# Performance work log

Hardware: AMD Instinct MI355X
Metric: run time of the kernel (lower is better)

## Reference

```python
import jax, jax.numpy as jnp
import numpy as np

B, T, C, V = 8, 2048, 1024, 32000


def setup_inputs() -> dict:
    key = jax.random.key(0)
    ks = jax.random.split(key, 12)
    s = 1.0 / np.sqrt(C)
    return {
        "input_tokens": jax.random.randint(ks[0], (B, T), 0, V),
        "xx_init": jnp.zeros((B, C), jnp.float32),
        "aa_init": jnp.zeros((B, C), jnp.float32),
        "bb_init": jnp.zeros((B, C), jnp.float32),
        "pp_init": jnp.zeros((B, C), jnp.float32),  # with aa=bb=0 this is equivalent to -inf init
        "emb": jax.random.normal(ks[1], (V, C), jnp.float32) * 0.02,
        "time_mix_k": jax.random.uniform(ks[2], (C,), jnp.float32),
        "time_mix_v": jax.random.uniform(ks[3], (C,), jnp.float32),
        "time_mix_r": jax.random.uniform(ks[4], (C,), jnp.float32),
        "time_decay": jax.random.normal(ks[5], (C,), jnp.float32) * 0.1,
        "time_first": jax.random.normal(ks[6], (C,), jnp.float32) * 0.1,
        "Wk": jax.random.normal(ks[7], (C, C), jnp.float32) * s,
        "Wv": jax.random.normal(ks[8], (C, C), jnp.float32) * s,
        "Wr": jax.random.normal(ks[9], (C, C), jnp.float32) * s,
        "Wo": jax.random.normal(ks[10], (C, C), jnp.float32) * s,
    }


def _wkv_scan(k, v, aa0, bb0, pp0, w, u):
    """Numerically-stable RWKV WKV recurrence.
    k, v: [T, B, C]; aa0/bb0/pp0: [B, C]; w (decay, negative), u (bonus): [C]."""
    def step(carry, kv):
        aa, bb, pp = carry
        kt, vt = kv
        ww = u + kt
        p = jnp.maximum(pp, ww)
        e1 = jnp.exp(pp - p)
        e2 = jnp.exp(ww - p)
        wkv = (e1 * aa + e2 * vt) / (e1 * bb + e2)
        ww2 = pp + w
        p2 = jnp.maximum(ww2, kt)
        e1b = jnp.exp(ww2 - p2)
        e2b = jnp.exp(kt - p2)
        return (e1b * aa + e2b * vt, e1b * bb + e2b, p2), wkv
    (aa, bb, pp), out = jax.lax.scan(step, (aa0, bb0, pp0), (k, v))
    return out, aa, bb, pp


def _forward(input_tokens, xx_init, aa_init, bb_init, pp_init, emb,
             time_mix_k, time_mix_v, time_mix_r, time_decay, time_first,
             Wk, Wv, Wr, Wo):
    x = emb[input_tokens]                                   # [B, T, C]
    xprev = jnp.concatenate([xx_init[:, None, :], x[:, :-1]], axis=1)  # token shift
    xk = x * time_mix_k + xprev * (1.0 - time_mix_k)
    xv = x * time_mix_v + xprev * (1.0 - time_mix_v)
    xr = x * time_mix_r + xprev * (1.0 - time_mix_r)
    k = jnp.einsum("btc,dc->btd", xk, Wk)
    v = jnp.einsum("btc,dc->btd", xv, Wv)
    r = jax.nn.sigmoid(jnp.einsum("btc,dc->btd", xr, Wr))
    w = -jnp.exp(time_decay)                                # per-channel decay
    u = time_first
    wkv, _, _, _ = _wkv_scan(jnp.swapaxes(k, 0, 1), jnp.swapaxes(v, 0, 1),
                             aa_init, bb_init, pp_init, w, u)
    wkv = jnp.swapaxes(wkv, 0, 1)                           # [B, T, C]
    rwkv = jnp.einsum("btc,dc->btd", r * wkv, Wo)
    e1 = rwkv[:, -1]          # final-step state
    e2 = rwkv.mean(axis=1)    # time-averaged state
    hx = (e1 + e2) * 0.5
    return jnp.stack([hx, hx])  # (hx, cx) stacked -> [2, B, C]


def reference(input_tokens, xx_init, aa_init, bb_init, pp_init, emb,
              time_mix_k, time_mix_v, time_mix_r, time_decay, time_first,
              Wk, Wv, Wr, Wo):
    return _forward(input_tokens, xx_init, aa_init, bb_init, pp_init, emb,
                    time_mix_k, time_mix_v, time_mix_r, time_decay, time_first,
                    Wk, Wv, Wr, Wo)
```

## Files before the change

kernel.cpp:

```cpp
#include <hip/hip_runtime.h>

#define Bdim 8
#define Tdim 2048
#define Cdim 1024
#define CHUNK 128
#define NCHUNK 16
#define BC (Bdim*Cdim)

typedef float floatx4 __attribute__((ext_vector_type(4)));
typedef _Float16 half8 __attribute__((ext_vector_type(8)));
typedef _Float16 half4v __attribute__((ext_vector_type(4)));

__device__ __forceinline__ void load16(const void* g, void* l) {
    __builtin_amdgcn_global_load_lds(
        (const __attribute__((address_space(1))) void*)g,
        (__attribute__((address_space(3))) void*)l, 16, 0, 0);
}

__global__ __launch_bounds__(256) void embed_mix(const int* __restrict__ tokens,
                                                 const float* __restrict__ xx_init,
                                                 const float* __restrict__ emb,
                                                 _Float16* __restrict__ xe) {
    int row = blockIdx.x;
    int b = row / (Tdim + 1);
    int tt = row % (Tdim + 1);
    const float* src;
    if (tt == 0) src = xx_init + (size_t)b * Cdim;
    else         src = emb + (size_t)tokens[b * Tdim + tt - 1] * Cdim;
    int c0 = threadIdx.x * 4;
    float4 f = *reinterpret_cast<const float4*>(src + c0);
    half4v h;
    h[0] = (_Float16)f.x; h[1] = (_Float16)f.y; h[2] = (_Float16)f.z; h[3] = (_Float16)f.w;
    *reinterpret_cast<half4v*>(xe + (size_t)row * Cdim + c0) = h;
}

__global__ __launch_bounds__(256) void mix3(const _Float16* __restrict__ xe,
                                            const float* __restrict__ tmk,
                                            const float* __restrict__ tmv,
                                            const float* __restrict__ tmr,
                                            _Float16* __restrict__ xk,
                                            _Float16* __restrict__ xv,
                                            _Float16* __restrict__ xr) {
    int row = blockIdx.x;
    int b = row >> 11;
    int t = row & (Tdim - 1);
    const _Float16* cur = xe + ((size_t)(b * (Tdim + 1) + t + 1)) * Cdim;
    const _Float16* prv = cur - Cdim;
    int c = threadIdx.x * 4;
    half4v cu = *reinterpret_cast<const half4v*>(cur + c);
    half4v pv = *reinterpret_cast<const half4v*>(prv + c);
    float4 mk = *reinterpret_cast<const float4*>(tmk + c);
    float4 mv = *reinterpret_cast<const float4*>(tmv + c);
    float4 mr = *reinterpret_cast<const float4*>(tmr + c);
    half4v hk, hv, hr;
    float cf[4] = {(float)cu[0], (float)cu[1], (float)cu[2], (float)cu[3]};
    float pf[4] = {(float)pv[0], (float)pv[1], (float)pv[2], (float)pv[3]};
    float mkf[4] = {mk.x, mk.y, mk.z, mk.w};
    float mvf[4] = {mv.x, mv.y, mv.z, mv.w};
    float mrf[4] = {mr.x, mr.y, mr.z, mr.w};
    #pragma unroll
    for (int j = 0; j < 4; j++) {
        hk[j] = (_Float16)(mkf[j] * cf[j] + (1.0f - mkf[j]) * pf[j]);
        hv[j] = (_Float16)(mvf[j] * cf[j] + (1.0f - mvf[j]) * pf[j]);
        hr[j] = (_Float16)(mrf[j] * cf[j] + (1.0f - mrf[j]) * pf[j]);
    }
    size_t o = (size_t)row * Cdim + c;
    *reinterpret_cast<half4v*>(xk + o) = hk;
    *reinterpret_cast<half4v*>(xv + o) = hv;
    *reinterpret_cast<half4v*>(xr + o) = hr;
}

__global__ __launch_bounds__(256) void wconv(const float* __restrict__ Wk,
                                             const float* __restrict__ Wv,
                                             const float* __restrict__ Wr,
                                             _Float16* __restrict__ Wh) {
    const float* W = blockIdx.y == 0 ? Wk : (blockIdx.y == 1 ? Wv : Wr);
    _Float16* dst = Wh + (size_t)blockIdx.y * Cdim * Cdim;
    int i = (blockIdx.x * 256 + threadIdx.x) * 4;
    float4 f = *reinterpret_cast<const float4*>(W + i);
    half4v h;
    h[0] = (_Float16)f.x; h[1] = (_Float16)f.y; h[2] = (_Float16)f.z; h[3] = (_Float16)f.w;
    *reinterpret_cast<half4v*>(dst + i) = h;
}

__global__ __launch_bounds__(256) void gemm_kvr(const _Float16* __restrict__ xk,
                                                const _Float16* __restrict__ xv,
                                                const _Float16* __restrict__ xr,
                                                const _Float16* __restrict__ Wh,
                                                _Float16* __restrict__ ko,
                                                _Float16* __restrict__ vo,
                                                _Float16* __restrict__ ro) {
    const int which = blockIdx.y;
    const _Float16* X = which == 0 ? xk : (which == 1 ? xv : xr);
    const _Float16* W = Wh + (size_t)which * Cdim * Cdim;
    _Float16* out     = which == 0 ? ko : (which == 1 ? vo : ro);

    const int lin = blockIdx.x;
    const int xcd = lin & 7;
    const int loc = lin >> 3;
    const int mt = xcd * 16 + (loc >> 3);
    const int nt = loc & 7;
    const int m0 = mt * 128;
    const int n0 = nt * 128;

    __shared__ _Float16 As[128 * 64];
    __shared__ _Float16 Bs[128 * 64];

    const int tid = threadIdx.x;
    const int lane = tid & 63;
    const int wave = tid >> 6;
    const int wm = (wave >> 1) * 64;
    const int wn = (wave & 1) * 64;
    const int lr = lane & 15;
    const int lk = lane >> 4;

    const _Float16* Asrc = X + (size_t)m0 * Cdim;
    const _Float16* Bsrc = W + (size_t)n0 * Cdim;

    floatx4 acc[4][4] = {};

    for (int k0 = 0; k0 < Cdim; k0 += 64) {
        #pragma unroll
        for (int i = 0; i < 4; i++) {
            int e = i * 256 + tid;
            int r = e >> 3;
            int cbp = e & 7;
            int cbl = cbp ^ (r & 7);
            load16(Asrc + (size_t)r * Cdim + k0 + cbl * 8, (char*)As + e * 16);
            load16(Bsrc + (size_t)r * Cdim + k0 + cbl * 8, (char*)Bs + e * 16);
        }
        __syncthreads();
        #pragma unroll
        for (int kk = 0; kk < 64; kk += 32) {
            const int kb_ = kk >> 3;
            half8 af[4], bf[4];
            #pragma unroll
            for (int mi = 0; mi < 4; mi++) {
                int r = wm + mi * 16 + lr;
                int cb = (kb_ + lk) ^ (r & 7);
                af[mi] = *reinterpret_cast<const half8*>(As + r * 64 + cb * 8);
            }
            #pragma unroll
            for (int ni = 0; ni < 4; ni++) {
                int r = wn + ni * 16 + lr;
                int cb = (kb_ + lk) ^ (r & 7);
                bf[ni] = *reinterpret_cast<const half8*>(Bs + r * 64 + cb * 8);
            }
            #pragma unroll
            for (int mi = 0; mi < 4; mi++)
                #pragma unroll
                for (int ni = 0; ni < 4; ni++)
                    acc[mi][ni] = __builtin_amdgcn_mfma_f32_16x16x32_f16(af[mi], bf[ni], acc[mi][ni], 0, 0, 0);
        }
        __syncthreads();
    }

    #pragma unroll
    for (int mi = 0; mi < 4; mi++) {
        #pragma unroll
        for (int ni = 0; ni < 4; ni++) {
            #pragma unroll
            for (int reg = 0; reg < 4; reg++) {
                int mm = m0 + wm + mi * 16 + (lane >> 4) * 4 + reg;
                int nn = n0 + wn + ni * 16 + (lane & 15);
                float v = acc[mi][ni][reg];
                if (which == 2) v = 1.0f / (1.0f + __expf(-v));
                out[(size_t)mm * Cdim + nn] = (_Float16)v;
            }
        }
    }
}

__global__ __launch_bounds__(256) void scan_pass1(const _Float16* __restrict__ kb,
                                                  const _Float16* __restrict__ vb,
                                                  const float* __restrict__ tdecay,
                                                  float* __restrict__ tot_a,
                                                  float* __restrict__ tot_b,
                                                  float* __restrict__ tot_p) {
    int idx = blockIdx.x * 256 + threadIdx.x;
    int j = idx >> 13;
    int bc = idx & (BC - 1);
    int b = bc >> 10;
    int c = bc & (Cdim - 1);
    float w = -__expf(tdecay[c]);
    float aa = 0.0f, bb = 0.0f, pp = -1e30f;
    const _Float16* kp = kb + ((size_t)(b * Tdim + j * CHUNK)) * Cdim + c;
    const _Float16* vp = vb + ((size_t)(b * Tdim + j * CHUNK)) * Cdim + c;
    #pragma unroll 4
    for (int t = 0; t < CHUNK; t++) {
        float kt = (float)kp[(size_t)t * Cdim];
        float vt = (float)vp[(size_t)t * Cdim];
        float ww2 = pp + w;
        float p2 = fmaxf(ww2, kt);
        float e1 = __expf(ww2 - p2);
        float e2 = __expf(kt - p2);
        aa = e1 * aa + e2 * vt;
        bb = e1 * bb + e2;
        pp = p2;
    }
    tot_a[idx] = aa; tot_b[idx] = bb; tot_p[idx] = pp;
}

__global__ __launch_bounds__(256) void combine_chunks(const float* __restrict__ tot_a,
                                                      const float* __restrict__ tot_b,
                                                      const float* __restrict__ tot_p,
                                                      const float* __restrict__ aa_init,
                                                      const float* __restrict__ bb_init,
                                                      const float* __restrict__ pp_init,
                                                      const float* __restrict__ tdecay,
                                                      float* __restrict__ inc_a,
                                                      float* __restrict__ inc_b,
                                                      float* __restrict__ inc_p) {
    int idx = blockIdx.x * 256 + threadIdx.x;
    int c = idx & (Cdim - 1);
    float w = -__expf(tdecay[c]);
    float wL = w * (float)CHUNK;
    float a = aa_init[idx], b = bb_init[idx], p = pp_init[idx];
    for (int j = 0; j < NCHUNK; j++) {
        inc_a[j * BC + idx] = a;
        inc_b[j * BC + idx] = b;
        inc_p[j * BC + idx] = p;
        float ta = tot_a[j * BC + idx];
        float tb = tot_b[j * BC + idx];
        float tp = tot_p[j * BC + idx];
        float px = p + wL;
        float q = fmaxf(px, tp);
        float e1 = __expf(px - q);
        float e2 = __expf(tp - q);
        a = e1 * a + e2 * ta;
        b = e1 * b + e2 * tb;
        p = q;
    }
}

__global__ __launch_bounds__(256) void scan_pass2(const _Float16* __restrict__ kb,
                                                  const _Float16* __restrict__ vb,
                                                  const _Float16* __restrict__ rb,
                                                  const float* __restrict__ tdecay,
                                                  const float* __restrict__ tfirst,
                                                  const float* __restrict__ inc_a,
                                                  const float* __restrict__ inc_b,
                                                  const float* __restrict__ inc_p,
                                                  float* __restrict__ partial,
                                                  float* __restrict__ ylast) {
    int idx = blockIdx.x * 256 + threadIdx.x;
    int j = idx >> 13;
    int bc = idx & (BC - 1);
    int b = bc >> 10;
    int c = bc & (Cdim - 1);
    float w = -__expf(tdecay[c]);
    float u = tfirst[c];
    float aa = inc_a[idx], bb = inc_b[idx], pp = inc_p[idx];
    const size_t base = ((size_t)(b * Tdim + j * CHUNK)) * Cdim + c;
    const _Float16* kp = kb + base;
    const _Float16* vp = vb + base;
    const _Float16* rp = rb + base;
    float sum = 0.0f, ylv = 0.0f;
    #pragma unroll 4
    for (int t = 0; t < CHUNK; t++) {
        float kt = (float)kp[(size_t)t * Cdim];
        float vt = (float)vp[(size_t)t * Cdim];
        float rt = (float)rp[(size_t)t * Cdim];
        float ww = u + kt;
        float p = fmaxf(pp, ww);
        float e1 = __expf(pp - p);
        float e2 = __expf(ww - p);
        float wkv = (e1 * aa + e2 * vt) / (e1 * bb + e2);
        float y = rt * wkv;
        sum += y;
        ylv = y;
        float ww2 = pp + w;
        float p2 = fmaxf(ww2, kt);
        float e1b = __expf(ww2 - p2);
        float e2b = __expf(kt - p2);
        aa = e1b * aa + e2b * vt;
        bb = e1b * bb + e2b;
        pp = p2;
    }
    partial[idx] = sum;
    if (j == NCHUNK - 1) ylast[bc] = ylv;
}

__global__ __launch_bounds__(256) void reduce_z(const float* __restrict__ partial,
                                                const float* __restrict__ ylast,
                                                float* __restrict__ z) {
    int idx = blockIdx.x * 256 + threadIdx.x;
    float s = 0.0f;
    for (int j = 0; j < NCHUNK; j++) s += partial[j * BC + idx];
    z[idx] = 0.5f * (ylast[idx] + s * (1.0f / (float)Tdim));
}

__global__ __launch_bounds__(256) void final_out(const float* __restrict__ z,
                                                 const float* __restrict__ Wo,
                                                 float* __restrict__ out) {
    int gw = (blockIdx.x * 256 + threadIdx.x) >> 6;
    int lane = threadIdx.x & 63;
    int b = gw >> 10;
    int d = gw & (Cdim - 1);
    const float* zr = z + (size_t)b * Cdim;
    const float* wr = Wo + (size_t)d * Cdim;
    float acc = 0.0f;
    #pragma unroll
    for (int i = lane; i < Cdim; i += 64) acc += zr[i] * wr[i];
    #pragma unroll
    for (int off = 32; off > 0; off >>= 1) acc += __shfl_down(acc, off);
    if (lane == 0) {
        out[(size_t)b * Cdim + d] = acc;
        out[(size_t)BC + (size_t)b * Cdim + d] = acc;
    }
}

extern "C" void kernel_launch(void* const* d_in, const int* in_sizes, int n_in,
                              void* d_out, int out_size, void* d_ws, size_t ws_size,
                              hipStream_t stream) {
    const int*   tokens  = (const int*)d_in[0];
    const float* xx_init = (const float*)d_in[1];
    const float* aa_init = (const float*)d_in[2];
    const float* bb_init = (const float*)d_in[3];
    const float* pp_init = (const float*)d_in[4];
    const float* emb     = (const float*)d_in[5];
    const float* tmk     = (const float*)d_in[6];
    const float* tmv     = (const float*)d_in[7];
    const float* tmr     = (const float*)d_in[8];
    const float* tdecay  = (const float*)d_in[9];
    const float* tfirst  = (const float*)d_in[10];
    const float* Wk      = (const float*)d_in[11];
    const float* Wv      = (const float*)d_in[12];
    const float* Wr      = (const float*)d_in[13];
    const float* Wo      = (const float*)d_in[14];
    float* out = (float*)d_out;

    char* ws = (char*)d_ws;
    size_t off = 0;
    auto alloc = [&](size_t bytes) -> void* {
        void* p = ws + off;
        off += (bytes + 255) & ~(size_t)255;
        return p;
    };
    _Float16* xe = (_Float16*)alloc((size_t)Bdim * (Tdim + 1) * Cdim * 2);
    _Float16* xkb = (_Float16*)alloc((size_t)Bdim * Tdim * Cdim * 2);
    _Float16* xvb = (_Float16*)alloc((size_t)Bdim * Tdim * Cdim * 2);
    _Float16* xrb = (_Float16*)alloc((size_t)Bdim * Tdim * Cdim * 2);
    _Float16* kb = xe;
    _Float16* vb = (_Float16*)alloc((size_t)Bdim * Tdim * Cdim * 2);
    _Float16* rb = (_Float16*)alloc((size_t)Bdim * Tdim * Cdim * 2);
    _Float16* Wh = (_Float16*)alloc((size_t)3 * Cdim * Cdim * 2);
    float* tot_a = (float*)alloc((size_t)NCHUNK * BC * 4);
    float* tot_b = (float*)alloc((size_t)NCHUNK * BC * 4);
    float* tot_p = (float*)alloc((size_t)NCHUNK * BC * 4);
    float* inc_a = (float*)alloc((size_t)NCHUNK * BC * 4);
    float* inc_b = (float*)alloc((size_t)NCHUNK * BC * 4);
    float* inc_p = (float*)alloc((size_t)NCHUNK * BC * 4);
    float* partial = (float*)alloc((size_t)NCHUNK * BC * 4);
    float* ylast   = (float*)alloc((size_t)BC * 4);
    float* zbuf    = (float*)alloc((size_t)BC * 4);

    embed_mix<<<Bdim * (Tdim + 1), 256, 0, stream>>>(tokens, xx_init, emb, xe);
    mix3<<<Bdim * Tdim, 256, 0, stream>>>(xe, tmk, tmv, tmr, xkb, xvb, xrb);
    wconv<<<dim3(1024, 3), 256, 0, stream>>>(Wk, Wv, Wr, Wh);
    gemm_kvr<<<dim3(1024, 3), 256, 0, stream>>>(xkb, xvb, xrb, Wh, kb, vb, rb);
    scan_pass1<<<(NCHUNK * BC) / 256, 256, 0, stream>>>(kb, vb, tdecay, tot_a, tot_b, tot_p);
    combine_chunks<<<BC / 256, 256, 0, stream>>>(tot_a, tot_b, tot_p, aa_init, bb_init, pp_init,
                                                 tdecay, inc_a, inc_b, inc_p);
    scan_pass2<<<(NCHUNK * BC) / 256, 256, 0, stream>>>(kb, vb, rb, tdecay, tfirst,
                                                        inc_a, inc_b, inc_p, partial, ylast);
    reduce_z<<<BC / 256, 256, 0, stream>>>(partial, ylast, zbuf);
    final_out<<<(BC / 4), 256, 0, stream>>>(zbuf, Wo, out);
}
```

Before: 419.0 us.

## Enlarge GEMM tiles to 256x256 with 4-stage async LDS pipeline

The k/v/r projection GEMM moves from 128x128 tiles with 256 threads and a load-sync-compute-sync loop to 256x256 tiles with 512 threads, K-step 32 and a four-buffer global-to-LDS pipeline. Loads for step kt+3 are issued before computing step kt, with manual vmcnt waits and a single barrier per step, plus setprio around the MFMA block. This is meant to hide global-load latency and raise arithmetic intensity per tile. It drops the XOR swizzle, so LDS bank conflicts may rise, uses 128KB of LDS and more registers per thread, and leaves fewer blocks for the CUs.

```diff
diff --git a/kernel.cpp b/kernel.cpp
--- a/kernel.cpp
+++ b/kernel.cpp
@@ -83,13 +83,13 @@
     *reinterpret_cast<half4v*>(dst + i) = h;
 }
 
-__global__ __launch_bounds__(256) void gemm_kvr(const _Float16* __restrict__ xk,
-                                                const _Float16* __restrict__ xv,
-                                                const _Float16* __restrict__ xr,
-                                                const _Float16* __restrict__ Wh,
-                                                _Float16* __restrict__ ko,
-                                                _Float16* __restrict__ vo,
-                                                _Float16* __restrict__ ro) {
+__global__ __launch_bounds__(512, 2) void gemm_kvr(const _Float16* __restrict__ xk,
+                                                   const _Float16* __restrict__ xv,
+                                                   const _Float16* __restrict__ xr,
+                                                   const _Float16* __restrict__ Wh,
+                                                   _Float16* __restrict__ ko,
+                                                   _Float16* __restrict__ vo,
+                                                   _Float16* __restrict__ ro) {
     const int which = blockIdx.y;
     const _Float16* X = which == 0 ? xk : (which == 1 ? xv : xr);
     const _Float16* W = Wh + (size_t)which * Cdim * Cdim;
@@ -98,65 +98,86 @@
     const int lin = blockIdx.x;
     const int xcd = lin & 7;
     const int loc = lin >> 3;
-    const int mt = xcd * 16 + (loc >> 3);
-    const int nt = loc & 7;
-    const int m0 = mt * 128;
-    const int n0 = nt * 128;
-
-    __shared__ _Float16 As[128 * 64];
-    __shared__ _Float16 Bs[128 * 64];
+    const int mt = xcd * 8 + (loc >> 2);
+    const int nt = loc & 3;
+    const int m0 = mt * 256;
+    const int n0 = nt * 256;
+
+    __shared__ _Float16 As[4 * 8192];
+    __shared__ _Float16 Bs[4 * 8192];
 
     const int tid = threadIdx.x;
     const int lane = tid & 63;
     const int wave = tid >> 6;
-    const int wm = (wave >> 1) * 64;
-    const int wn = (wave & 1) * 64;
+    const int wm = (wave >> 2) * 128;
+    const int wn = (wave & 3) * 64;
     const int lr = lane & 15;
     const int lk = lane >> 4;
 
     const _Float16* Asrc = X + (size_t)m0 * Cdim;
     const _Float16* Bsrc = W + (size_t)n0 * Cdim;
 
-    floatx4 acc[4][4] = {};
-
-    for (int k0 = 0; k0 < Cdim; k0 += 64) {
-        #pragma unroll
-        for (int i = 0; i < 4; i++) {
-            int e = i * 256 + tid;
-            int r = e >> 3;
-            int cbp = e & 7;
-            int cbl = cbp ^ (r & 7);
-            load16(Asrc + (size_t)r * Cdim + k0 + cbl * 8, (char*)As + e * 16);
-            load16(Bsrc + (size_t)r * Cdim + k0 + cbl * 8, (char*)Bs + e * 16);
+    floatx4 acc[8][4] = {};
+
+    auto stage = [&](int kt) {
+        const int p = kt & 3;
+        const int k0 = kt * 32;
+        #pragma unroll
+        for (int i = 0; i < 2; i++) {
+            int e = i * 512 + tid;
+            int r = e >> 2;
+            int s = e & 3;
+            load16(Asrc + (size_t)r * Cdim + k0 + s * 8, (char*)(As + p * 8192) + e * 16);
         }
-        __syncthreads();
-        #pragma unroll
-        for (int kk = 0; kk < 64; kk += 32) {
-            const int kb_ = kk >> 3;
-            half8 af[4], bf[4];
+        #pragma unroll
+        for (int i = 0; i < 2; i++) {
+            int e = i * 512 + tid;
+            int r = e >> 2;
+            int s = e & 3;
+            load16(Bsrc + (size_t)r * Cdim + k0 + s * 8, (char*)(Bs + p * 8192) + e * 16);
+        }
+    };
+
+    auto compute = [&](int kt) {
+        const int p = kt & 3;
+        const _Float16* ap = As + p * 8192 + (wm + lr) * 32 + lk * 8;
+        const _Float16* bp = Bs + p * 8192 + (wn + lr) * 32 + lk * 8;
+        half8 af[8], bf[4];
+        #pragma unroll
+        for (int mi = 0; mi < 8; mi++)
+            af[mi] = *reinterpret_cast<const half8*>(ap + mi * 16 * 32);
+        #pragma unroll
+        for (int ni = 0; ni < 4; ni++)
+            bf[ni] = *reinterpret_cast<const half8*>(bp + ni * 16 * 32);
+        __builtin_amdgcn_s_setprio(1);
+        #pragma unroll
+        for (int mi = 0; mi < 8; mi++)
             #pragma unroll
-            for (int mi = 0; mi < 4; mi++) {
-                int r = wm + mi * 16 + lr;
-                int cb = (kb_ + lk) ^ (r & 7);
-                af[mi] = *reinterpret_cast<const half8*>(As + r * 64 + cb * 8);
-            }
-            #pragma unroll
-            for (int ni = 0; ni < 4; ni++) {
-                int r = wn + ni * 16 + lr;
-                int cb = (kb_ + lk) ^ (r & 7);
-                bf[ni] = *reinterpret_cast<const half8*>(Bs + r * 64 + cb * 8);
-            }
-            #pragma unroll
-            for (int mi = 0; mi < 4; mi++)
-                #pragma unroll
-                for (int ni = 0; ni < 4; ni++)
-                    acc[mi][ni] = __builtin_amdgcn_mfma_f32_16x16x32_f16(af[mi], bf[ni], acc[mi][ni], 0, 0, 0);
-        }
-        __syncthreads();
-    }
+            for (int ni = 0; ni < 4; ni++)
+                acc[mi][ni] = __builtin_amdgcn_mfma_f32_16x16x32_f16(af[mi], bf[ni], acc[mi][ni], 0, 0, 0);
+        __builtin_amdgcn_s_setprio(0);
+    };
+
+    stage(0); stage(1); stage(2);
+    asm volatile("s_waitcnt vmcnt(8)" ::: "memory");
+    __builtin_amdgcn_s_barrier();
+
+    for (int kt = 0; kt < 29; ++kt) {
+        stage(kt + 3);
+        compute(kt);
+        asm volatile("s_waitcnt vmcnt(8)" ::: "memory");
+        __builtin_amdgcn_s_barrier();
+    }
+    compute(29);
+    asm volatile("s_waitcnt vmcnt(4)" ::: "memory");
+    __builtin_amdgcn_s_barrier();
+    compute(30);
+    asm volatile("s_waitcnt vmcnt(0)" ::: "memory");
+    __builtin_amdgcn_s_barrier();
+    compute(31);
 
     #pragma unroll
-    for (int mi = 0; mi < 4; mi++) {
+    for (int mi = 0; mi < 8; mi++) {
         #pragma unroll
         for (int ni = 0; ni < 4; ni++) {
             #pragma unroll
@@ -358,7 +379,7 @@
     embed_mix<<<Bdim * (Tdim + 1), 256, 0, stream>>>(tokens, xx_init, emb, xe);
     mix3<<<Bdim * Tdim, 256, 0, stream>>>(xe, tmk, tmv, tmr, xkb, xvb, xrb);
     wconv<<<dim3(1024, 3), 256, 0, stream>>>(Wk, Wv, Wr, Wh);
-    gemm_kvr<<<dim3(1024, 3), 256, 0, stream>>>(xkb, xvb, xrb, Wh, kb, vb, rb);
+    gemm_kvr<<<dim3(256, 3), 512, 0, stream>>>(xkb, xvb, xrb, Wh, kb, vb, rb);
     scan_pass1<<<(NCHUNK * BC) / 256, 256, 0, stream>>>(kb, vb, tdecay, tot_a, tot_b, tot_p);
     combine_chunks<<<BC / 256, 256, 0, stream>>>(tot_a, tot_b, tot_p, aa_init, bb_init, pp_init,
                                                  tdecay, inc_a, inc_b, inc_p);
```

Measured after the change: 416.4 us. Within noise of the previous version (-0.6%).
